# Optimization experiments

Hardware: AMD Instinct MI355X
Metric: run time of the kernel (lower is better)

## Reference

```python
import jax, jax.numpy as jnp
import numpy as np

EMBED_DIM = 1024
NUM_HEADS = 16
HEAD_DIM = EMBED_DIM // NUM_HEADS
B, S = 4, 2048


def setup_inputs() -> dict:
    key = jax.random.key(0)
    k1, k2, k3, k4, k5 = jax.random.split(key, 5)
    x = jax.random.normal(k1, (B, S, EMBED_DIM), dtype=jnp.float32)
    # torch nn.Linear params: W [out, in], b [out]; init scale ~ 1/sqrt(in)
    s = 1.0 / np.sqrt(EMBED_DIM)
    qkv_w = jax.random.uniform(k2, (3 * EMBED_DIM, EMBED_DIM), jnp.float32, -s, s)
    qkv_b = jax.random.uniform(k3, (3 * EMBED_DIM,), jnp.float32, -s, s)
    out_w = jax.random.uniform(k4, (EMBED_DIM, EMBED_DIM), jnp.float32, -s, s)
    out_b = jax.random.uniform(k5, (EMBED_DIM,), jnp.float32, -s, s)
    return {"x": x, "qkv_w": qkv_w, "qkv_b": qkv_b, "out_w": out_w, "out_b": out_b}


def reference(x, qkv_w, qkv_b, out_w, out_b):
    b, s, e = x.shape
    # qkv: [B,S,3E]
    qkv = x @ qkv_w.T + qkv_b
    # Faithful to source: reshape to [B,S,H,3*hd] then transpose -> [B,H,S,3*hd]
    qkv = qkv.reshape(b, s, NUM_HEADS, 3 * HEAD_DIM).transpose(0, 2, 1, 3)
    q, k, v = jnp.split(qkv, 3, axis=-1)  # each [B,H,S,hd]
    q = q / np.sqrt(HEAD_DIM).astype(np.float32)
    scores = jnp.einsum('bhqd,bhkd->bhqk', q, k)  # [B,H,S,S]
    attn = jax.nn.softmax(scores, axis=-1)
    out = jnp.einsum('bhqk,bhkd->bhqd', attn, v)  # [B,H,S,hd]
    out = out.transpose(0, 2, 1, 3).reshape(b, s, e)
    return out @ out_w.T + out_b
```

## Files before the change

kernel.cpp:

```cpp
#include <hip/hip_runtime.h>

#define EMBED   1024
#define THREE_E 3072
#define NHEAD   16
#define HDIM    64
#define BATCH   4
#define SEQ     2048
#define MTOK    (BATCH * SEQ)
#define QKW     2048

typedef __attribute__((ext_vector_type(8)))  _Float16 half8;
typedef __attribute__((ext_vector_type(4)))  _Float16 half4;
typedef __attribute__((ext_vector_type(4)))  float    f32x4;
typedef __attribute__((ext_vector_type(4)))  unsigned uint4v;

#define QSCALE 0.18033688011112042f

__device__ inline f32x4 mfma16(half8 a, half8 b, f32x4 c) {
    return __builtin_amdgcn_mfma_f32_16x16x32_f16(a, b, c, 0, 0, 0);
}

__device__ inline float exp2x(float x) {
    float r;
    asm("v_exp_f32 %0, %1" : "=v"(r) : "v"(x));
    return r;
}
__device__ inline unsigned pk2(float a, float b) {
    return __builtin_bit_cast(unsigned, __builtin_amdgcn_cvt_pkrtz(a, b));
}

__device__ inline void gld16(const void* g, void* l) {
    __builtin_amdgcn_global_load_lds(
        (const __attribute__((address_space(1))) unsigned*)g,
        (__attribute__((address_space(3))) unsigned*)l, 16, 0, 0);
}

__global__ __launch_bounds__(256) void tohi3_kernel(
    const float* __restrict__ x,  _Float16* __restrict__ xo,
    const float* __restrict__ w1, _Float16* __restrict__ w1o,
    const float* __restrict__ w2, _Float16* __restrict__ w2o)
{
    const int bid = blockIdx.x;
    const float* src; _Float16* dst; int base;
    if (bid < 8192)             { src = x;  dst = xo;  base = bid * 1024; }
    else if (bid < 8192 + 3072) { src = w1; dst = w1o; base = (bid - 8192) * 1024; }
    else                        { src = w2; dst = w2o; base = (bid - 11264) * 1024; }
    const int i = base + (threadIdx.x << 2);
    const float4 v = *(const float4*)(src + i);
    half4 h;
    h[0] = (_Float16)v.x; h[1] = (_Float16)v.y;
    h[2] = (_Float16)v.z; h[3] = (_Float16)v.w;
    *(half4*)(dst + i) = h;
}

template<int OMODE>
__global__ __launch_bounds__(512, 2) void gemm_big(
    const _Float16* __restrict__ Ahi,
    const _Float16* __restrict__ Bhi,
    const float*  __restrict__ bias,
    float* __restrict__ Cf,
    _Float16* __restrict__ QKhi,
    _Float16* __restrict__ Vthi,
    int N, int K)
{
    __shared__ __align__(16) _Float16 sA[3][8][2][64][8];
    __shared__ __align__(16) _Float16 sB[3][16][2][64][8];

    const int tid  = threadIdx.x;
    const int w    = tid >> 6;
    const int lane = tid & 63;
    const int quad = lane >> 4;
    const int c    = lane & 15;
    const int wr   = w >> 2, wc = w & 3;

    const int gx   = gridDim.x;
    const int nwg  = gx * gridDim.y;
    const int lin0 = blockIdx.y * gx + blockIdx.x;
    const int wg   = (lin0 & 7) * (nwg >> 3) + (lin0 >> 3);
    const int m0   = (wg / gx) << 7;
    const int n0   = (wg % gx) << 8;

    f32x4 acc[4][4];
#pragma unroll
    for (int i = 0; i < 4; ++i)
#pragma unroll
        for (int j = 0; j < 4; ++j) acc[i][j] = (f32x4){0.f, 0.f, 0.f, 0.f};

    const int rg0 = w >> 1, ksb = w & 1;
    const size_t sK64 = (size_t)64 * K;
    const _Float16* ap = Ahi + (size_t)(m0 + rg0 * 16 + c) * K + ksb * 32 + quad * 8;
    const _Float16* bp = Bhi + (size_t)(n0 + rg0 * 16 + c) * K + ksb * 32 + quad * 8;

    auto stage_p0 = [&](int sl) {
        gld16(ap,            &sA[sl][rg0][ksb][0][0]);
        gld16(ap + sK64,     &sA[sl][4 + rg0][ksb][0][0]);
        gld16(bp,            &sB[sl][rg0][ksb][0][0]);
    };
    auto stage_p1 = [&](int sl) {
        gld16(bp + sK64,     &sB[sl][4 + rg0][ksb][0][0]);
        gld16(bp + 2 * sK64, &sB[sl][8 + rg0][ksb][0][0]);
        gld16(bp + 3 * sK64, &sB[sl][12 + rg0][ksb][0][0]);
        ap += 64; bp += 64;
    };

    stage_p0(0); stage_p1(0);
    stage_p0(1); stage_p1(1);

    const int NT = K >> 6;
    int slot = 0;
    for (int t = 0; t < NT; ++t) {
        if (t + 1 < NT) { asm volatile("s_waitcnt vmcnt(6)" ::: "memory"); }
        else            { asm volatile("s_waitcnt vmcnt(0)" ::: "memory"); }
        __builtin_amdgcn_s_barrier();

        const bool pre = (t + 2) < NT;
        int ns = slot + 2; if (ns >= 3) ns -= 3;

        half8 aH[4][2], bH[4][2];
#pragma unroll
        for (int fr = 0; fr < 4; ++fr)
#pragma unroll
            for (int ks = 0; ks < 2; ++ks)
                aH[fr][ks] = *(const half8*)&sA[slot][wr * 4 + fr][ks][lane][0];
#pragma unroll
        for (int fc = 0; fc < 2; ++fc)
#pragma unroll
            for (int ks = 0; ks < 2; ++ks)
                bH[fc][ks] = *(const half8*)&sB[slot][wc * 4 + fc][ks][lane][0];
        if (pre) stage_p0(ns);
        __builtin_amdgcn_s_setprio(1);
#pragma unroll
        for (int fr = 0; fr < 4; ++fr)
#pragma unroll
            for (int fc = 0; fc < 2; ++fc)
#pragma unroll
                for (int ks = 0; ks < 2; ++ks)
                    acc[fr][fc] = mfma16(aH[fr][ks], bH[fc][ks], acc[fr][fc]);
        __builtin_amdgcn_s_setprio(0);
        __builtin_amdgcn_s_barrier();

#pragma unroll
        for (int fc = 2; fc < 4; ++fc)
#pragma unroll
            for (int ks = 0; ks < 2; ++ks)
                bH[fc][ks] = *(const half8*)&sB[slot][wc * 4 + fc][ks][lane][0];
        if (pre) stage_p1(ns);
        __builtin_amdgcn_s_setprio(1);
#pragma unroll
        for (int fr = 0; fr < 4; ++fr)
#pragma unroll
            for (int fc = 2; fc < 4; ++fc)
#pragma unroll
                for (int ks = 0; ks < 2; ++ks)
                    acc[fr][fc] = mfma16(aH[fr][ks], bH[fc][ks], acc[fr][fc]);
        __builtin_amdgcn_s_setprio(0);

        slot = (slot == 2) ? 0 : slot + 1;
    }

#pragma unroll
    for (int fc = 0; fc < 4; ++fc) {
        const int n  = n0 + wc * 64 + fc * 16 + c;
        const float bb = bias[n];
        const int h  = n / 192;
        const int rem = n - h * 192;
#pragma unroll
        for (int fr = 0; fr < 4; ++fr) {
            const int mb = m0 + wr * 64 + fr * 16 + (quad << 2);
            if constexpr (OMODE == 0) {
#pragma unroll
                for (int r = 0; r < 4; ++r)
                    Cf[(size_t)(mb + r) * N + n] = acc[fr][fc][r] + bb;
            } else {
                if (rem < 128) {
                    const size_t col = h * 128 + rem;
                    const float scale = (rem < 64) ? QSCALE : 1.0f;
#pragma unroll
                    for (int r = 0; r < 4; ++r)
                        QKhi[(size_t)(mb + r) * QKW + col] =
                            (_Float16)((acc[fr][fc][r] + bb) * scale);
                } else {
                    const int d  = rem - 128;
                    const int b  = mb >> 11;
                    const int s  = mb & 2047;
                    const int kt = s >> 6;
                    const int rs = s & 63;
                    const int gp = rs >> 5;
                    const int hf = (rs >> 4) & 1;
                    const int kq = (rs >> 2) & 3;
                    const int v  = d >> 4;
                    const int cl = d & 15;
                    half4 h4;
#pragma unroll
                    for (int r = 0; r < 4; ++r)
                        h4[r] = (_Float16)(acc[fr][fc][r] + bb);
                    const size_t off =
                        ((((size_t)(h * BATCH + b) * (SEQ / 64) + kt) * 8
                          + (v * 2 + gp)) * 512)
                        + (size_t)(kq * 16 + cl) * 8 + hf * 4;
                    *(half4*)(Vthi + off) = h4;
                }
            }
        }
    }
}

__global__ __launch_bounds__(256, 4) void attn_mfma(
    const _Float16* __restrict__ qkhi,
    const _Float16* __restrict__ vthi,
    _Float16* __restrict__ attnf)
{
    __shared__ __align__(16) _Float16 Kf[2][8][512];
    __shared__ __align__(16) _Float16 Vf[2][8][512];

    const int tid  = threadIdx.x;
    const int w    = tid >> 6;
    const int lane = tid & 63;
    const int quad = lane >> 4;
    const int c    = lane & 15;

    const int lin = blockIdx.x;
    const int g   = lin & 7;
    const int s   = lin >> 3;
    const int bh  = g * 8 + (s >> 4);
    const int qt  = s & 15;
    const int b   = bh >> 4, h = bh & 15;
    const int q0  = qt * 128;

    const size_t bSEQ  = (size_t)b * SEQ;
    const int    qcol  = h * 128;
    const int    kcol  = h * 128 + 64;

    half8 qh[2][2];
#pragma unroll
    for (int t = 0; t < 2; ++t) {
        const size_t row = (bSEQ + q0 + w * 32 + t * 16 + c) * QKW;
#pragma unroll
        for (int ks = 0; ks < 2; ++ks)
            qh[t][ks] = *(const half8*)(qkhi + row + qcol + ks * 32 + quad * 8);
    }

    f32x4 lacc[2];
    f32x4 oacc[4][2];
#pragma unroll
    for (int t = 0; t < 2; ++t) {
        lacc[t] = (f32x4){0.f, 0.f, 0.f, 0.f};
#pragma unroll
        for (int v = 0; v < 4; ++v) oacc[v][t] = (f32x4){0.f, 0.f, 0.f, 0.f};
    }

    const half8 one8 = {(_Float16)1.f, (_Float16)1.f, (_Float16)1.f, (_Float16)1.f,
                        (_Float16)1.f, (_Float16)1.f, (_Float16)1.f, (_Float16)1.f};

    const int ku0 = w >> 1,       kks0 = w & 1;
    const int ku1 = (4 + w) >> 1, kks1 = (4 + w) & 1;
    const _Float16* kp0 = qkhi + (bSEQ + ku0 * 16 + c) * QKW + kcol + kks0 * 32 + quad * 8;
    const _Float16* kp1 = qkhi + (bSEQ + ku1 * 16 + c) * QKW + kcol + kks1 * 32 + quad * 8;
    const _Float16* vp0 = vthi + ((size_t)(h * BATCH + b) * (SEQ / 64)) * 4096
                               + (size_t)w * 512 + lane * 8;
    const _Float16* vp1 = vp0 + 4 * 512;

    auto stageKV = [&](int bfs) {
        gld16(kp0, &Kf[bfs][w][0]);
        gld16(kp1, &Kf[bfs][4 + w][0]);
        gld16(vp0, &Vf[bfs][w][0]);
        gld16(vp1, &Vf[bfs][4 + w][0]);
        kp0 += 64 * QKW; kp1 += 64 * QKW; vp0 += 4096; vp1 += 4096;
    };

    stageKV(0);
    int bf = 0;

    for (int kt = 0; kt < SEQ / 64; ++kt) {
        __syncthreads();
        if (kt + 1 < SEQ / 64) stageKV(bf ^ 1);

        f32x4 sacc[2][4];
        __builtin_amdgcn_s_setprio(1);
#pragma unroll
        for (int u = 0; u < 4; ++u) {
            const half8 kh0 = *(const half8*)&Kf[bf][(u << 1) + 0][lane << 3];
            const half8 kh1 = *(const half8*)&Kf[bf][(u << 1) + 1][lane << 3];
#pragma unroll
            for (int t = 0; t < 2; ++t) {
                f32x4 a = (f32x4){0.f, 0.f, 0.f, 0.f};
                a = mfma16(kh0, qh[t][0], a);
                a = mfma16(kh1, qh[t][1], a);
                sacc[t][u] = a;
            }
        }
        __builtin_amdgcn_s_setprio(0);

        half8 pb[2][2];
#pragma unroll
        for (int t = 0; t < 2; ++t)
#pragma unroll
            for (int gp = 0; gp < 2; ++gp) {
                uint4v wd;
#pragma unroll
                for (int hf = 0; hf < 2; ++hf) {
                    const int u = 2 * gp + hf;
                    const float p0 = exp2x(sacc[t][u][0]);
                    const float p1 = exp2x(sacc[t][u][1]);
                    const float p2 = exp2x(sacc[t][u][2]);
                    const float p3 = exp2x(sacc[t][u][3]);
                    if (hf == 0) { wd.x = pk2(p0, p1); wd.y = pk2(p2, p3); }
                    else         { wd.z = pk2(p0, p1); wd.w = pk2(p2, p3); }
                }
                pb[t][gp] = __builtin_bit_cast(half8, wd);
            }

        half8 vb[4][2];
#pragma unroll
        for (int v = 0; v < 4; ++v)
#pragma unroll
            for (int gp = 0; gp < 2; ++gp)
                vb[v][gp] = *(const half8*)&Vf[bf][(v << 1) + gp][lane << 3];

        __builtin_amdgcn_s_setprio(1);
#pragma unroll
        for (int t = 0; t < 2; ++t) {
#pragma unroll
            for (int v = 0; v < 4; ++v) {
                f32x4 a = oacc[v][t];
                a = mfma16(vb[v][0], pb[t][0], a);
                a = mfma16(vb[v][1], pb[t][1], a);
                oacc[v][t] = a;
            }
            f32x4 l = lacc[t];
            l = mfma16(one8, pb[t][0], l);
            l = mfma16(one8, pb[t][1], l);
            lacc[t] = l;
        }
        __builtin_amdgcn_s_setprio(0);

        bf ^= 1;
    }

#pragma unroll
    for (int t = 0; t < 2; ++t) {
        const float inv = 1.0f / lacc[t][0];
        const int tok = q0 + w * 32 + t * 16 + c;
#pragma unroll
        for (int v = 0; v < 4; ++v) {
            half4 o;
#pragma unroll
            for (int r = 0; r < 4; ++r) o[r] = (_Float16)(oacc[v][t][r] * inv);
            *(half4*)&attnf[(bSEQ + tok) * EMBED + h * HDIM + v * 16 + (quad << 2)] = o;
        }
    }
}

extern "C" void kernel_launch(void* const* d_in, const int* in_sizes, int n_in,
                              void* d_out, int out_size, void* d_ws, size_t ws_size,
                              hipStream_t stream)
{
    const float* x     = (const float*)d_in[0];
    const float* qkv_w = (const float*)d_in[1];
    const float* qkv_b = (const float*)d_in[2];
    const float* out_w = (const float*)d_in[3];
    const float* out_b = (const float*)d_in[4];

    _Float16* qkhi  = (_Float16*)d_ws;
    _Float16* vthi  = qkhi  + (size_t)MTOK * QKW;
    _Float16* w1hi  = vthi  + (size_t)NHEAD * HDIM * BATCH * SEQ;
    _Float16* w2hi  = w1hi  + (size_t)THREE_E * EMBED;
    _Float16* attnf = w2hi  + (size_t)EMBED * EMBED;

    _Float16* xhi = (_Float16*)d_out;

    tohi3_kernel<<<dim3(12288), 256, 0, stream>>>(x, xhi, qkv_w, w1hi, out_w, w2hi);

    gemm_big<1><<<dim3(THREE_E / 256, MTOK / 128), 512, 0, stream>>>(
        xhi, w1hi, qkv_b, nullptr, qkhi, vthi, THREE_E, EMBED);

    attn_mfma<<<dim3(1024), 256, 0, stream>>>(qkhi, vthi, attnf);

    gemm_big<0><<<dim3(EMBED / 256, MTOK / 128), 512, 0, stream>>>(
        attnf, w2hi, out_b, (float*)d_out, nullptr, nullptr, EMBED, EMBED);
}
```

Before: 276.2 us.

## Halve GEMM K-tile to 32 and raise occupancy target to 4 blocks

Shrinks the per-stage K tile in the big GEMM from 64 to 32, which halves the shared-memory footprint of the triple buffer. It simplifies staging to one load phase per iteration with a single barrier, and raises launch bounds to 4 blocks per CU. This aims for more resident waves to hide latency, but it doubles the number of loop iterations and barriers per K and tightens the register budget, which could cause spills.

```diff
diff --git a/kernel.cpp b/kernel.cpp
--- a/kernel.cpp
+++ b/kernel.cpp
@@ -54,7 +54,7 @@
 }
 
 template<int OMODE>
-__global__ __launch_bounds__(512, 2) void gemm_big(
+__global__ __launch_bounds__(512, 4) void gemm_big(
     const _Float16* __restrict__ Ahi,
     const _Float16* __restrict__ Bhi,
     const float*  __restrict__ bias,
@@ -63,8 +63,8 @@
     _Float16* __restrict__ Vthi,
     int N, int K)
 {
-    __shared__ __align__(16) _Float16 sA[3][8][2][64][8];
-    __shared__ __align__(16) _Float16 sB[3][16][2][64][8];
+    __shared__ __align__(16) _Float16 sA[3][8][64][8];
+    __shared__ __align__(16) _Float16 sB[3][16][64][8];
 
     const int tid  = threadIdx.x;
     const int w    = tid >> 6;
@@ -86,73 +86,45 @@
 #pragma unroll
         for (int j = 0; j < 4; ++j) acc[i][j] = (f32x4){0.f, 0.f, 0.f, 0.f};
 
-    const int rg0 = w >> 1, ksb = w & 1;
-    const size_t sK64 = (size_t)64 * K;
-    const _Float16* ap = Ahi + (size_t)(m0 + rg0 * 16 + c) * K + ksb * 32 + quad * 8;
-    const _Float16* bp = Bhi + (size_t)(n0 + rg0 * 16 + c) * K + ksb * 32 + quad * 8;
-
-    auto stage_p0 = [&](int sl) {
-        gld16(ap,            &sA[sl][rg0][ksb][0][0]);
-        gld16(ap + sK64,     &sA[sl][4 + rg0][ksb][0][0]);
-        gld16(bp,            &sB[sl][rg0][ksb][0][0]);
+    const _Float16* ap  = Ahi + (size_t)(m0 + w * 16 + c) * K + quad * 8;
+    const _Float16* bp0 = Bhi + (size_t)(n0 + w * 16 + c) * K + quad * 8;
+    const _Float16* bp8 = Bhi + (size_t)(n0 + 128 + w * 16 + c) * K + quad * 8;
+
+    auto stage = [&](int sl) {
+        gld16(ap,  &sA[sl][w][0][0]);
+        gld16(bp0, &sB[sl][w][0][0]);
+        gld16(bp8, &sB[sl][8 + w][0][0]);
+        ap += 32; bp0 += 32; bp8 += 32;
     };
-    auto stage_p1 = [&](int sl) {
-        gld16(bp + sK64,     &sB[sl][4 + rg0][ksb][0][0]);
-        gld16(bp + 2 * sK64, &sB[sl][8 + rg0][ksb][0][0]);
-        gld16(bp + 3 * sK64, &sB[sl][12 + rg0][ksb][0][0]);
-        ap += 64; bp += 64;
-    };
-
-    stage_p0(0); stage_p1(0);
-    stage_p0(1); stage_p1(1);
-
-    const int NT = K >> 6;
+
+    stage(0); stage(1);
+
+    const int NT = K >> 5;
     int slot = 0;
     for (int t = 0; t < NT; ++t) {
-        if (t + 1 < NT) { asm volatile("s_waitcnt vmcnt(6)" ::: "memory"); }
+        if (t + 1 < NT) { asm volatile("s_waitcnt vmcnt(3)" ::: "memory"); }
         else            { asm volatile("s_waitcnt vmcnt(0)" ::: "memory"); }
         __builtin_amdgcn_s_barrier();
 
-        const bool pre = (t + 2) < NT;
-        int ns = slot + 2; if (ns >= 3) ns -= 3;
-
-        half8 aH[4][2], bH[4][2];
+        if (t + 2 < NT) {
+            int ns = slot + 2; if (ns >= 3) ns -= 3;
+            stage(ns);
+        }
+
+        half8 aH[4], bH[4];
 #pragma unroll
         for (int fr = 0; fr < 4; ++fr)
-#pragma unroll
-            for (int ks = 0; ks < 2; ++ks)
-                aH[fr][ks] = *(const half8*)&sA[slot][wr * 4 + fr][ks][lane][0];
-#pragma unroll
-        for (int fc = 0; fc < 2; ++fc)
-#pragma unroll
-            for (int ks = 0; ks < 2; ++ks)
-                bH[fc][ks] = *(const half8*)&sB[slot][wc * 4 + fc][ks][lane][0];
-        if (pre) stage_p0(ns);
+            aH[fr] = *(const half8*)&sA[slot][wr * 4 + fr][lane][0];
+#pragma unroll
+        for (int fc = 0; fc < 4; ++fc)
+            bH[fc] = *(const half8*)&sB[slot][wc * 4 + fc][lane][0];
+
         __builtin_amdgcn_s_setprio(1);
 #pragma unroll
         for (int fr = 0; fr < 4; ++fr)
 #pragma unroll
-            for (int fc = 0; fc < 2; ++fc)
-#pragma unroll
-                for (int ks = 0; ks < 2; ++ks)
-                    acc[fr][fc] = mfma16(aH[fr][ks], bH[fc][ks], acc[fr][fc]);
-        __builtin_amdgcn_s_setprio(0);
-        __builtin_amdgcn_s_barrier();
-
-#pragma unroll
-        for (int fc = 2; fc < 4; ++fc)
-#pragma unroll
-            for (int ks = 0; ks < 2; ++ks)
-                bH[fc][ks] = *(const half8*)&sB[slot][wc * 4 + fc][ks][lane][0];
-        if (pre) stage_p1(ns);
-        __builtin_amdgcn_s_setprio(1);
-#pragma unroll
-        for (int fr = 0; fr < 4; ++fr)
-#pragma unroll
-            for (int fc = 2; fc < 4; ++fc)
-#pragma unroll
-                for (int ks = 0; ks < 2; ++ks)
-                    acc[fr][fc] = mfma16(aH[fr][ks], bH[fc][ks], acc[fr][fc]);
+            for (int fc = 0; fc < 4; ++fc)
+                acc[fr][fc] = mfma16(aH[fr], bH[fc], acc[fr][fc]);
         __builtin_amdgcn_s_setprio(0);
 
         slot = (slot == 2) ? 0 : slot + 1;
```

Result: slower. 301.2 us (+9.1%).
